# Kernel optimization log

Hardware: AMD Instinct MI355X
Metric: run time of the kernel (lower is better)

## Reference

```python
import jax, jax.numpy as jnp
import numpy as np

N_EMBD = 1024
HEAD_SIZE = 64


def setup_inputs() -> dict:
    key = jax.random.key(0)
    ks = jax.random.split(key, 7)
    B, T, C, H = 4, 4096, N_EMBD, HEAD_SIZE
    s = 1.0 / np.sqrt(C)
    return {
        "x": jax.random.normal(ks[0], (B, T, C), dtype=jnp.float32),
        "Wk": jax.random.uniform(ks[1], (C, H), jnp.float32, -s, s),
        "bk": jax.random.uniform(ks[2], (H,), jnp.float32, -s, s),
        "Wq": jax.random.uniform(ks[3], (C, H), jnp.float32, -s, s),
        "bq": jax.random.uniform(ks[4], (H,), jnp.float32, -s, s),
        "Wv": jax.random.uniform(ks[5], (C, H), jnp.float32, -s, s),
        "bv": jax.random.uniform(ks[6], (H,), jnp.float32, -s, s),
    }


def reference(x, Wk, bk, Wq, bq, Wv, bv):
    B, T, C = x.shape
    k = x @ Wk + bk  # [B,T,H]
    q = x @ Wq + bq
    v = x @ Wv + bv
    scale = k.shape[-1] ** -0.5
    wei = jnp.einsum("bth,bsh->bts", q, k) * scale  # [B,T,T]
    causal = jnp.tril(jnp.ones((T, T), dtype=bool))
    wei = jnp.where(causal, wei, -jnp.inf)
    wei = jax.nn.softmax(wei, axis=-1)
    return jnp.einsum("bts,bsh->bth", wei, v)
```

## Files before the change

### kernel.cpp

```cpp
#include <hip/hip_runtime.h>
#include <hip/hip_bf16.h>


typedef _Float16 f16;
typedef f16 half4 __attribute__((ext_vector_type(4)));
typedef f16 half8 __attribute__((ext_vector_type(8)));
typedef float f32x4 __attribute__((ext_vector_type(4)));

#define T_SEQ 4096

__device__ __forceinline__ f32x4 mfma16(half8 a, half8 b, f32x4 c) {
    return __builtin_amdgcn_mfma_f32_16x16x32_f16(a, b, c, 0, 0, 0);
}

__global__ __launch_bounds__(256) void prep_w(const float* __restrict__ Wq,
                                              const float* __restrict__ Wk,
                                              const float* __restrict__ Wv,
                                              f16* __restrict__ Wfrag) {
    int nt = blockIdx.x;
    int mat = nt >> 2;
    const float* W = (mat == 0) ? Wq : (mat == 1 ? Wk : Wv);
    float s = (mat == 0) ? 0.125f : 1.0f;
    int tid = threadIdx.x;
    int lane = tid & 63, g = lane >> 4, c16 = lane & 15;
    int ksb = (tid >> 6) * 8;
    int h = ((nt & 3) << 4) + c16;
#pragma unroll
    for (int q = 0; q < 8; ++q) {
        int ks = ksb + q;
        half8 o;
#pragma unroll
        for (int j = 0; j < 8; ++j) {
            int k = ks * 32 + g * 8 + j;
            o[j] = (f16)(W[(size_t)k * 64 + h] * s);
        }
        *reinterpret_cast<half8*>(&Wfrag[((size_t)(nt * 32 + ks) * 64 + lane) * 8]) = o;
    }
}

__global__ __launch_bounds__(256, 4) void proj(const float* __restrict__ x,
                                               const f16* __restrict__ Wfrag,
                                               const float* __restrict__ bk,
                                               const float* __restrict__ bq,
                                               const float* __restrict__ bv,
                                               f16* __restrict__ Qb, f16* __restrict__ Kb,
                                               f16* __restrict__ Vbt) {
    __shared__ f16 xs[16][1032];
    int m0 = blockIdx.x << 4;
    int tid = threadIdx.x;
    int w = tid >> 6, lane = tid & 63, g = lane >> 4, c16 = lane & 15;

    {
        int row = tid >> 4;
        int c0 = (tid & 15) << 2;
        const float* xr = &x[(size_t)(m0 + row) * 1024 + c0];
#pragma unroll
        for (int chunk = 0; chunk < 8; ++chunk) {
            float4 A = *reinterpret_cast<const float4*>(xr + chunk * 128);
            float4 B = *reinterpret_cast<const float4*>(xr + chunk * 128 + 64);
            half4 ha, hb;
            ha[0] = (f16)A.x; ha[1] = (f16)A.y; ha[2] = (f16)A.z; ha[3] = (f16)A.w;
            hb[0] = (f16)B.x; hb[1] = (f16)B.y; hb[2] = (f16)B.z; hb[3] = (f16)B.w;
            *reinterpret_cast<half4*>(&xs[row][c0 + chunk * 128]) = ha;
            *reinterpret_cast<half4*>(&xs[row][c0 + chunk * 128 + 64]) = hb;
        }
    }
    __syncthreads();

    f32x4 zero = {0.f, 0.f, 0.f, 0.f};
    f32x4 acc[3];
#pragma unroll
    for (int i = 0; i < 3; ++i) acc[i] = zero;
    const f16* wbase = &Wfrag[(size_t)(w * 3) * 32 * 64 * 8 + (size_t)lane * 8];
#pragma unroll 8
    for (int ks = 0; ks < 32; ++ks) {
        half8 a = *reinterpret_cast<const half8*>(&xs[c16][ks * 32 + g * 8]);
#pragma unroll
        for (int i = 0; i < 3; ++i) {
            half8 bf = *reinterpret_cast<const half8*>(
                wbase + ((size_t)i * 32 + ks) * 64 * 8);
            acc[i] = mfma16(a, bf, acc[i]);
        }
    }
    int b = m0 >> 12;
#pragma unroll
    for (int i = 0; i < 3; ++i) {
        int nt = w * 3 + i;
        int mat = nt >> 2;
        int h = ((nt & 3) << 4) + c16;
        float bias = (mat == 0) ? bq[h] * 0.125f : (mat == 1 ? bk[h] : bv[h]);
#pragma unroll
        for (int j = 0; j < 4; ++j) {
            int row = m0 + g * 4 + j;
            f16 val = (f16)(acc[i][j] + bias);
            if (mat == 0) Qb[(size_t)row * 64 + h] = val;
            else if (mat == 1) Kb[(size_t)row * 64 + h] = val;
            else Vbt[((size_t)(b * 64 + h)) * 4096 + (row & 4095)] = val;
        }
    }
}

__global__ __launch_bounds__(256) void attn(const f16* __restrict__ Qb,
                                            const f16* __restrict__ Kb,
                                            const f16* __restrict__ Vbt,
                                            f16* __restrict__ Opart,
                                            float* __restrict__ Ml) {
    int qt = blockIdx.x, b = blockIdx.y, ck = blockIdx.z;
    int t0 = ck << 4;
    if (t0 > qt) return;
    int nT = min(t0 + 16, qt + 1);
    int nIter = nT - t0;
    int q0 = qt << 6;
    const f16* Q = Qb + (size_t)b * T_SEQ * 64;
    const f16* K = Kb + (size_t)b * T_SEQ * 64;
    const f16* Vg = Vbt + (size_t)b * 64 * T_SEQ;
    int tid = threadIdx.x;
    int w = tid >> 6, lane = tid & 63, g = lane >> 4, c16 = lane & 15;
    __shared__ f16 Kt[2][64][72];
    __shared__ f16 Vt[2][64][72];
    __shared__ f16 Pl[4][16][72];

    half8 qf0 = *reinterpret_cast<const half8*>(&Q[(size_t)(q0 + 16 * w + c16) * 64 + g * 8]);
    half8 qf1 = *reinterpret_cast<const half8*>(&Q[(size_t)(q0 + 16 * w + c16) * 64 + 32 + g * 8]);

    f32x4 zero = {0.f, 0.f, 0.f, 0.f};
    f32x4 oacc[4];
#pragma unroll
    for (int i = 0; i < 4; ++i) oacc[i] = zero;
    float m_run[4], l_run[4];
#pragma unroll
    for (int j = 0; j < 4; ++j) { m_run[j] = -__builtin_inff(); l_run[j] = 0.f; }

    int sr = tid >> 2, sc = (tid & 3) << 4;
    int k0 = t0 << 6;
    half8 kr0 = *reinterpret_cast<const half8*>(&K[(size_t)(k0 + sr) * 64 + sc]);
    half8 kr1 = *reinterpret_cast<const half8*>(&K[(size_t)(k0 + sr) * 64 + sc + 8]);
    half8 vr0 = *reinterpret_cast<const half8*>(&Vg[(size_t)sr * T_SEQ + k0 + sc]);
    half8 vr1 = *reinterpret_cast<const half8*>(&Vg[(size_t)sr * T_SEQ + k0 + sc + 8]);
    *reinterpret_cast<half8*>(&Kt[0][sr][sc]) = kr0;
    *reinterpret_cast<half8*>(&Kt[0][sr][sc + 8]) = kr1;
    *reinterpret_cast<half8*>(&Vt[0][sr][sc]) = vr0;
    *reinterpret_cast<half8*>(&Vt[0][sr][sc + 8]) = vr1;
    __syncthreads();
    int cur = 0;

    for (int it = 0; it < nIter; ++it) {
        int gt = t0 + it;
        if (it + 1 < nIter) {
            int kn = (gt + 1) << 6;
            kr0 = *reinterpret_cast<const half8*>(&K[(size_t)(kn + sr) * 64 + sc]);
            kr1 = *reinterpret_cast<const half8*>(&K[(size_t)(kn + sr) * 64 + sc + 8]);
            vr0 = *reinterpret_cast<const half8*>(&Vg[(size_t)sr * T_SEQ + kn + sc]);
            vr1 = *reinterpret_cast<const half8*>(&Vg[(size_t)sr * T_SEQ + kn + sc + 8]);
        }
        f32x4 s[4];
#pragma unroll
        for (int nt = 0; nt < 4; ++nt) s[nt] = zero;
#pragma unroll
        for (int nt = 0; nt < 4; ++nt) {
            half8 b0 = *reinterpret_cast<const half8*>(&Kt[cur][nt * 16 + c16][g * 8]);
            half8 b1 = *reinterpret_cast<const half8*>(&Kt[cur][nt * 16 + c16][32 + g * 8]);
            s[nt] = mfma16(qf0, b0, s[nt]);
            s[nt] = mfma16(qf1, b1, s[nt]);
        }
        if (gt == qt) {
            int kb = gt << 6;
#pragma unroll
            for (int nt = 0; nt < 4; ++nt)
#pragma unroll
                for (int j = 0; j < 4; ++j)
                    if (kb + nt * 16 + c16 > q0 + 16 * w + g * 4 + j) s[nt][j] = -1e30f;
        }
        float mx[4];
#pragma unroll
        for (int j = 0; j < 4; ++j)
            mx[j] = fmaxf(fmaxf(s[0][j], s[1][j]), fmaxf(s[2][j], s[3][j]));
#pragma unroll
        for (int off = 1; off < 16; off <<= 1)
#pragma unroll
            for (int j = 0; j < 4; ++j) mx[j] = fmaxf(mx[j], __shfl_xor(mx[j], off, 64));
        float al[4];
#pragma unroll
        for (int j = 0; j < 4; ++j) {
            float nm = fmaxf(m_run[j], mx[j]);
            al[j] = __expf(m_run[j] - nm);
            m_run[j] = nm;
        }
        float pm[4][4];
#pragma unroll
        for (int nt = 0; nt < 4; ++nt)
#pragma unroll
            for (int j = 0; j < 4; ++j) pm[nt][j] = __expf(s[nt][j] - m_run[j]);
        float rs[4];
#pragma unroll
        for (int j = 0; j < 4; ++j) rs[j] = pm[0][j] + pm[1][j] + pm[2][j] + pm[3][j];
#pragma unroll
        for (int off = 1; off < 16; off <<= 1)
#pragma unroll
            for (int j = 0; j < 4; ++j) rs[j] += __shfl_xor(rs[j], off, 64);
#pragma unroll
        for (int j = 0; j < 4; ++j) l_run[j] = l_run[j] * al[j] + rs[j];
#pragma unroll
        for (int ht = 0; ht < 4; ++ht)
#pragma unroll
            for (int j = 0; j < 4; ++j) oacc[ht][j] *= al[j];
#pragma unroll
        for (int nt = 0; nt < 4; ++nt)
#pragma unroll
            for (int j = 0; j < 4; ++j) Pl[w][g * 4 + j][nt * 16 + c16] = (f16)pm[nt][j];
        half8 pa0 = *reinterpret_cast<const half8*>(&Pl[w][c16][g * 8]);
        half8 pa1 = *reinterpret_cast<const half8*>(&Pl[w][c16][32 + g * 8]);
#pragma unroll
        for (int ht = 0; ht < 4; ++ht) {
            half8 vb0 = *reinterpret_cast<const half8*>(&Vt[cur][ht * 16 + c16][g * 8]);
            half8 vb1 = *reinterpret_cast<const half8*>(&Vt[cur][ht * 16 + c16][32 + g * 8]);
            oacc[ht] = mfma16(pa0, vb0, oacc[ht]);
            oacc[ht] = mfma16(pa1, vb1, oacc[ht]);
        }
        if (it + 1 < nIter) {
            *reinterpret_cast<half8*>(&Kt[cur ^ 1][sr][sc]) = kr0;
            *reinterpret_cast<half8*>(&Kt[cur ^ 1][sr][sc + 8]) = kr1;
            *reinterpret_cast<half8*>(&Vt[cur ^ 1][sr][sc]) = vr0;
            *reinterpret_cast<half8*>(&Vt[cur ^ 1][sr][sc + 8]) = vr1;
        }
        __syncthreads();
        cur ^= 1;
    }
    int slot = (((b << 6) + qt) << 2) + ck;
    f16* Op = Opart + (size_t)slot * 4096;
    float* mlp = Ml + (size_t)slot * 128;
#pragma unroll
    for (int j = 0; j < 4; ++j) {
        int r = 16 * w + g * 4 + j;
#pragma unroll
        for (int ht = 0; ht < 4; ++ht)
            Op[r * 64 + ht * 16 + c16] = (f16)oacc[ht][j];
        if (c16 == 0) { mlp[r] = m_run[j]; mlp[64 + r] = l_run[j]; }
    }
}

__global__ __launch_bounds__(256) void combine(const f16* __restrict__ Opart,
                                               const float* __restrict__ Ml,
                                               float* __restrict__ out) {
    int qt = blockIdx.x, b = blockIdx.y;
    int nck = (qt >> 4) + 1;
    int tid = threadIdx.x;
    int row = tid >> 2, c0 = (tid & 3) << 4;
    int bslot = ((b << 6) + qt) << 2;
    float mv[4], lv[4];
    float M = -1e30f;
#pragma unroll
    for (int i = 0; i < 4; ++i)
        if (i < nck) {
            mv[i] = Ml[(size_t)(bslot + i) * 128 + row];
            lv[i] = Ml[(size_t)(bslot + i) * 128 + 64 + row];
            M = fmaxf(M, mv[i]);
        }
    float L = 0.f, sc[4];
#pragma unroll
    for (int i = 0; i < 4; ++i)
        if (i < nck) { sc[i] = __expf(mv[i] - M); L += lv[i] * sc[i]; }
    float inv = 1.0f / L;
    float o[16];
#pragma unroll
    for (int j = 0; j < 16; ++j) o[j] = 0.f;
#pragma unroll
    for (int i = 0; i < 4; ++i)
        if (i < nck) {
            const f16* Op = Opart + (size_t)(bslot + i) * 4096 + row * 64 + c0;
            half8 h0 = *reinterpret_cast<const half8*>(Op);
            half8 h1 = *reinterpret_cast<const half8*>(Op + 8);
#pragma unroll
            for (int j = 0; j < 8; ++j) {
                o[j] += sc[i] * (float)h0[j];
                o[8 + j] += sc[i] * (float)h1[j];
            }
        }
    float* op = &out[((size_t)b * T_SEQ + (qt << 6) + row) * 64 + c0];
#pragma unroll
    for (int j = 0; j < 16; ++j) op[j] = o[j] * inv;
}

extern "C" void kernel_launch(void* const* d_in, const int* in_sizes, int n_in,
                              void* d_out, int out_size, void* d_ws, size_t ws_size,
                              hipStream_t stream) {
    (void)in_sizes; (void)n_in; (void)out_size; (void)ws_size;
    const float* x  = (const float*)d_in[0];
    const float* Wk = (const float*)d_in[1];
    const float* bk = (const float*)d_in[2];
    const float* Wq = (const float*)d_in[3];
    const float* bq = (const float*)d_in[4];
    const float* Wv = (const float*)d_in[5];
    const float* bv = (const float*)d_in[6];
    float* out = (float*)d_out;
    char* ws = (char*)d_ws;
    f16* Wfrag = (f16*)(ws);
    f16* Qb    = (f16*)(ws + 393216);
    f16* Kb    = (f16*)(ws + 393216 + 2097152);
    f16* Vbt   = (f16*)(ws + 393216 + 2 * 2097152);
    f16* Opart = (f16*)(ws + 393216 + 3 * 2097152);
    float* Ml  = (float*)(ws + 393216 + 3 * 2097152 + 8388608);

    prep_w<<<12, 256, 0, stream>>>(Wq, Wk, Wv, Wfrag);
    proj<<<1024, 256, 0, stream>>>(x, Wfrag, bk, bq, bv, Qb, Kb, Vbt);
    attn<<<dim3(64, 4, 4), 256, 0, stream>>>(Qb, Kb, Vbt, Opart, Ml);
    combine<<<dim3(64, 4), 256, 0, stream>>>(Opart, Ml, out);
}
```

Baseline: 167.8 us.

## Transpose score MFMA so each lane owns one query row, use exp2 softmax

Swaps the MFMA operand order for QK^T and PV so the accumulator holds S^T. Each lane then owns a single query row, and the row max and sum need only two cross-group shuffles instead of four-step butterflies across four rows. The log2(e) factor is folded into the Q scaling so exp2f can replace __expf. P and O are written as packed half4 vectors, and the query-tile launch order is reversed so the heavy tiles are scheduled first. This touches the masking index logic and the combine step, which must stay consistent with the base-2 running max.

```diff
diff --git a/kernel.cpp b/kernel.cpp
--- a/kernel.cpp
+++ b/kernel.cpp
@@ -8,6 +8,7 @@
 typedef float f32x4 __attribute__((ext_vector_type(4)));
 
 #define T_SEQ 4096
+#define QSCL 0.1803368801111204f
 
 __device__ __forceinline__ f32x4 mfma16(half8 a, half8 b, f32x4 c) {
     return __builtin_amdgcn_mfma_f32_16x16x32_f16(a, b, c, 0, 0, 0);
@@ -20,7 +21,7 @@
     int nt = blockIdx.x;
     int mat = nt >> 2;
     const float* W = (mat == 0) ? Wq : (mat == 1 ? Wk : Wv);
-    float s = (mat == 0) ? 0.125f : 1.0f;
+    float s = (mat == 0) ? QSCL : 1.0f;
     int tid = threadIdx.x;
     int lane = tid & 63, g = lane >> 4, c16 = lane & 15;
     int ksb = (tid >> 6) * 8;
@@ -49,7 +50,6 @@
     int m0 = blockIdx.x << 4;
     int tid = threadIdx.x;
     int w = tid >> 6, lane = tid & 63, g = lane >> 4, c16 = lane & 15;
-
     {
         int row = tid >> 4;
         int c0 = (tid & 15) << 2;
@@ -66,7 +66,6 @@
         }
     }
     __syncthreads();
-
     f32x4 zero = {0.f, 0.f, 0.f, 0.f};
     f32x4 acc[3];
 #pragma unroll
@@ -88,7 +87,7 @@
         int nt = w * 3 + i;
         int mat = nt >> 2;
         int h = ((nt & 3) << 4) + c16;
-        float bias = (mat == 0) ? bq[h] * 0.125f : (mat == 1 ? bk[h] : bv[h]);
+        float bias = (mat == 0) ? bq[h] * QSCL : (mat == 1 ? bk[h] : bv[h]);
 #pragma unroll
         for (int j = 0; j < 4; ++j) {
             int row = m0 + g * 4 + j;
@@ -105,7 +104,8 @@
                                             const f16* __restrict__ Vbt,
                                             f16* __restrict__ Opart,
                                             float* __restrict__ Ml) {
-    int qt = blockIdx.x, b = blockIdx.y, ck = blockIdx.z;
+    int qt = 63 - blockIdx.x;
+    int b = blockIdx.y, ck = blockIdx.z;
     int t0 = ck << 4;
     if (t0 > qt) return;
     int nT = min(t0 + 16, qt + 1);
@@ -127,9 +127,7 @@
     f32x4 oacc[4];
 #pragma unroll
     for (int i = 0; i < 4; ++i) oacc[i] = zero;
-    float m_run[4], l_run[4];
-#pragma unroll
-    for (int j = 0; j < 4; ++j) { m_run[j] = -__builtin_inff(); l_run[j] = 0.f; }
+    float m_run = -__builtin_inff(), l_run = 0.f;
 
     int sr = tid >> 2, sc = (tid & 3) << 4;
     int k0 = t0 << 6;
@@ -153,69 +151,74 @@
             vr0 = *reinterpret_cast<const half8*>(&Vg[(size_t)sr * T_SEQ + kn + sc]);
             vr1 = *reinterpret_cast<const half8*>(&Vg[(size_t)sr * T_SEQ + kn + sc + 8]);
         }
-        f32x4 s[4];
-#pragma unroll
-        for (int nt = 0; nt < 4; ++nt) s[nt] = zero;
+        f32x4 st[4];
+#pragma unroll
+        for (int nt = 0; nt < 4; ++nt) st[nt] = zero;
 #pragma unroll
         for (int nt = 0; nt < 4; ++nt) {
-            half8 b0 = *reinterpret_cast<const half8*>(&Kt[cur][nt * 16 + c16][g * 8]);
-            half8 b1 = *reinterpret_cast<const half8*>(&Kt[cur][nt * 16 + c16][32 + g * 8]);
-            s[nt] = mfma16(qf0, b0, s[nt]);
-            s[nt] = mfma16(qf1, b1, s[nt]);
+            half8 kf0 = *reinterpret_cast<const half8*>(&Kt[cur][nt * 16 + c16][g * 8]);
+            half8 kf1 = *reinterpret_cast<const half8*>(&Kt[cur][nt * 16 + c16][32 + g * 8]);
+            st[nt] = mfma16(kf0, qf0, st[nt]);
+            st[nt] = mfma16(kf1, qf1, st[nt]);
         }
         if (gt == qt) {
             int kb = gt << 6;
+            int qr = q0 + 16 * w + c16;
 #pragma unroll
             for (int nt = 0; nt < 4; ++nt)
 #pragma unroll
-                for (int j = 0; j < 4; ++j)
-                    if (kb + nt * 16 + c16 > q0 + 16 * w + g * 4 + j) s[nt][j] = -1e30f;
-        }
-        float mx[4];
-#pragma unroll
-        for (int j = 0; j < 4; ++j)
-            mx[j] = fmaxf(fmaxf(s[0][j], s[1][j]), fmaxf(s[2][j], s[3][j]));
-#pragma unroll
-        for (int off = 1; off < 16; off <<= 1)
-#pragma unroll
-            for (int j = 0; j < 4; ++j) mx[j] = fmaxf(mx[j], __shfl_xor(mx[j], off, 64));
-        float al[4];
-#pragma unroll
-        for (int j = 0; j < 4; ++j) {
-            float nm = fmaxf(m_run[j], mx[j]);
-            al[j] = __expf(m_run[j] - nm);
-            m_run[j] = nm;
-        }
+                for (int jj = 0; jj < 4; ++jj)
+                    if (kb + nt * 16 + g * 4 + jj > qr) st[nt][jj] = -1e30f;
+        }
+        float m01, m23, mx;
+        {
+            f32x4 a = st[0], bq4 = st[1], c = st[2], d = st[3];
+            f32x4 e;
+            e[0] = fmaxf(fmaxf(a[0], a[1]), fmaxf(a[2], a[3]));
+            e[1] = fmaxf(fmaxf(bq4[0], bq4[1]), fmaxf(bq4[2], bq4[3]));
+            e[2] = fmaxf(fmaxf(c[0], c[1]), fmaxf(c[2], c[3]));
+            e[3] = fmaxf(fmaxf(d[0], d[1]), fmaxf(d[2], d[3]));
+            m01 = fmaxf(e[0], e[1]); m23 = fmaxf(e[2], e[3]);
+            mx = fmaxf(m01, m23);
+        }
+        mx = fmaxf(mx, __shfl_xor(mx, 16, 64));
+        mx = fmaxf(mx, __shfl_xor(mx, 32, 64));
+        float nm = fmaxf(m_run, mx);
+        float al = exp2f(m_run - nm);
+        m_run = nm;
         float pm[4][4];
-#pragma unroll
-        for (int nt = 0; nt < 4; ++nt)
-#pragma unroll
-            for (int j = 0; j < 4; ++j) pm[nt][j] = __expf(s[nt][j] - m_run[j]);
-        float rs[4];
-#pragma unroll
-        for (int j = 0; j < 4; ++j) rs[j] = pm[0][j] + pm[1][j] + pm[2][j] + pm[3][j];
-#pragma unroll
-        for (int off = 1; off < 16; off <<= 1)
-#pragma unroll
-            for (int j = 0; j < 4; ++j) rs[j] += __shfl_xor(rs[j], off, 64);
-#pragma unroll
-        for (int j = 0; j < 4; ++j) l_run[j] = l_run[j] * al[j] + rs[j];
+        float rs = 0.f;
+#pragma unroll
+        for (int nt = 0; nt < 4; ++nt) {
+            float s0 = exp2f(st[nt][0] - m_run);
+            float s1 = exp2f(st[nt][1] - m_run);
+            float s2 = exp2f(st[nt][2] - m_run);
+            float s3 = exp2f(st[nt][3] - m_run);
+            pm[nt][0] = s0; pm[nt][1] = s1; pm[nt][2] = s2; pm[nt][3] = s3;
+            rs += (s0 + s1) + (s2 + s3);
+        }
+        rs += __shfl_xor(rs, 16, 64);
+        rs += __shfl_xor(rs, 32, 64);
+        l_run = l_run * al + rs;
 #pragma unroll
         for (int ht = 0; ht < 4; ++ht)
 #pragma unroll
-            for (int j = 0; j < 4; ++j) oacc[ht][j] *= al[j];
-#pragma unroll
-        for (int nt = 0; nt < 4; ++nt)
-#pragma unroll
-            for (int j = 0; j < 4; ++j) Pl[w][g * 4 + j][nt * 16 + c16] = (f16)pm[nt][j];
+            for (int jj = 0; jj < 4; ++jj) oacc[ht][jj] *= al;
+#pragma unroll
+        for (int nt = 0; nt < 4; ++nt) {
+            half4 p4;
+            p4[0] = (f16)pm[nt][0]; p4[1] = (f16)pm[nt][1];
+            p4[2] = (f16)pm[nt][2]; p4[3] = (f16)pm[nt][3];
+            *reinterpret_cast<half4*>(&Pl[w][c16][nt * 16 + g * 4]) = p4;
+        }
         half8 pa0 = *reinterpret_cast<const half8*>(&Pl[w][c16][g * 8]);
         half8 pa1 = *reinterpret_cast<const half8*>(&Pl[w][c16][32 + g * 8]);
 #pragma unroll
         for (int ht = 0; ht < 4; ++ht) {
             half8 vb0 = *reinterpret_cast<const half8*>(&Vt[cur][ht * 16 + c16][g * 8]);
             half8 vb1 = *reinterpret_cast<const half8*>(&Vt[cur][ht * 16 + c16][32 + g * 8]);
-            oacc[ht] = mfma16(pa0, vb0, oacc[ht]);
-            oacc[ht] = mfma16(pa1, vb1, oacc[ht]);
+            oacc[ht] = mfma16(vb0, pa0, oacc[ht]);
+            oacc[ht] = mfma16(vb1, pa1, oacc[ht]);
         }
         if (it + 1 < nIter) {
             *reinterpret_cast<half8*>(&Kt[cur ^ 1][sr][sc]) = kr0;
@@ -229,14 +232,15 @@
     int slot = (((b << 6) + qt) << 2) + ck;
     f16* Op = Opart + (size_t)slot * 4096;
     float* mlp = Ml + (size_t)slot * 128;
-#pragma unroll
-    for (int j = 0; j < 4; ++j) {
-        int r = 16 * w + g * 4 + j;
-#pragma unroll
-        for (int ht = 0; ht < 4; ++ht)
-            Op[r * 64 + ht * 16 + c16] = (f16)oacc[ht][j];
-        if (c16 == 0) { mlp[r] = m_run[j]; mlp[64 + r] = l_run[j]; }
-    }
+    int r = 16 * w + c16;
+#pragma unroll
+    for (int ht = 0; ht < 4; ++ht) {
+        half4 o4;
+        o4[0] = (f16)oacc[ht][0]; o4[1] = (f16)oacc[ht][1];
+        o4[2] = (f16)oacc[ht][2]; o4[3] = (f16)oacc[ht][3];
+        *reinterpret_cast<half4*>(&Op[r * 64 + ht * 16 + g * 4]) = o4;
+    }
+    if (g == 0) { mlp[r] = m_run; mlp[64 + r] = l_run; }
 }
 
 __global__ __launch_bounds__(256) void combine(const f16* __restrict__ Opart,
@@ -259,7 +263,7 @@
     float L = 0.f, sc[4];
 #pragma unroll
     for (int i = 0; i < 4; ++i)
-        if (i < nck) { sc[i] = __expf(mv[i] - M); L += lv[i] * sc[i]; }
+        if (i < nck) { sc[i] = exp2f(mv[i] - M); L += lv[i] * sc[i]; }
     float inv = 1.0f / L;
     float o[16];
 #pragma unroll
```

Measured after the change: 159.2 us. -5.1%, faster.
